# Performance work log

Hardware: AMD Instinct MI355X
Metric: run time of the kernel (lower is better)

## Reference

```python
import jax, jax.numpy as jnp
import numpy as np

B, N, D = 2, 1024, 1024
H, DH = 16, 64          # nhead, head_dim (D = H*DH)
FF = 4096               # dim_feedforward = 4*D
E = 8                   # num experts
EPS = 1e-5


def layer_norm(x, s, b):
    m = jnp.mean(x, -1, keepdims=True)
    v = jnp.mean((x - m) ** 2, -1, keepdims=True)
    return (x - m) * jax.lax.rsqrt(v + EPS) * s + b


def moe_gate(x, Wg):
    # top-1 gating: expert index + gate probability per token
    probs = jax.nn.softmax(x @ Wg, axis=-1)            # [B,N,E]
    idx = jnp.argmax(probs, axis=-1)                   # [B,N]
    gw = jnp.take_along_axis(probs, idx[..., None], -1)[..., 0]  # [B,N]
    return idx, gw


def moe_linear(x, W, b, idx, gw):
    # x:[B,N,Din], W:[E,Din,Dout], b:[E,Dout]; route each token to expert idx
    y = jnp.einsum('bnd,edh->bneh', x, W) + b          # [B,N,E,Dout]
    oh = jax.nn.one_hot(idx, E, dtype=x.dtype)         # [B,N,E]
    return jnp.einsum('bneh,bne->bnh', y, oh) * gw[..., None]


def setup_inputs() -> dict:
    key = jax.random.key(0)
    ks = jax.random.split(key, 8)
    g = lambda k, shape, sc: jax.random.normal(k, shape, jnp.float32) * sc
    inv_d = 1.0 / np.sqrt(D)
    return dict(
        src=g(ks[0], (B, N, D), 1.0),
        key_padding_mask=jnp.zeros((B, N), dtype=bool),
        Wg_attn=g(ks[1], (D, E), inv_d),
        Wqkv=g(ks[2], (E, D, 3 * D), inv_d), bqkv=jnp.zeros((E, 3 * D), jnp.float32),
        Wo=g(ks[3], (E, D, D), inv_d), bo=jnp.zeros((E, D), jnp.float32),
        Wg_ffn=g(ks[4], (D, E), inv_d),
        W1=g(ks[5], (E, D, FF), inv_d), b1=jnp.zeros((E, FF), jnp.float32),
        W2=g(ks[6], (E, FF, D), 1.0 / np.sqrt(FF)), b2=jnp.zeros((E, D), jnp.float32),
        ln1_s=jnp.ones((D,), jnp.float32), ln1_b=jnp.zeros((D,), jnp.float32),
        ln2_s=jnp.ones((D,), jnp.float32), ln2_b=jnp.zeros((D,), jnp.float32),
    )


def reference(src, key_padding_mask, Wg_attn, Wqkv, bqkv, Wo, bo,
              Wg_ffn, W1, b1, W2, b2, ln1_s, ln1_b, ln2_s, ln2_b):
    # attention mask: key_padding_mask.unsqueeze(1).unsqueeze(1) * -10000
    mask = jnp.where(key_padding_mask[:, None, None, :], -10000.0, 0.0).astype(src.dtype)

    # --- MoE self-attention (gate decided once, reused for qkv and dense) ---
    idx, gw = moe_gate(src, Wg_attn)
    qkv = moe_linear(src, Wqkv, bqkv, idx, gw)                 # [B,N,3D]
    q, k, v = jnp.split(qkv, 3, axis=-1)
    heads = lambda t: t.reshape(B, N, H, DH).transpose(0, 2, 1, 3)  # [B,H,N,DH]
    q, k, v = heads(q), heads(k), heads(v)
    scores = jnp.einsum('bhqd,bhkd->bhqk', q, k) / np.sqrt(DH) + mask
    probs = jax.nn.softmax(scores, axis=-1)
    ctx = jnp.einsum('bhqk,bhkd->bhqd', probs, v)
    ctx = ctx.transpose(0, 2, 1, 3).reshape(B, N, D)
    attn_out = moe_linear(ctx, Wo, bo, idx, gw)

    # post-norm residual
    x = layer_norm(src + attn_out, ln1_s, ln1_b)

    # --- MoE FFN (its own gate, shared across both linears) ---
    fidx, fgw = moe_gate(x, Wg_ffn)
    h = jax.nn.gelu(moe_linear(x, W1, b1, fidx, fgw))
    ffn = moe_linear(h, W2, b2, fidx, fgw)

    return layer_norm(x + ffn, ln2_s, ln2_b)
```

## Files before the change

### kernel.cpp

```cpp
#include <hip/hip_runtime.h>


#define B_   2
#define N_   1024
#define D_   1024
#define H_   16
#define DH_  64
#define FF_  4096
#define E_   8
#define NTOK 2048

typedef __attribute__((ext_vector_type(8))) short short8;
typedef __attribute__((ext_vector_type(8))) unsigned short ushort8;
typedef __attribute__((ext_vector_type(4))) unsigned short ushort4v;
typedef __attribute__((ext_vector_type(4))) float f32x4;
typedef __attribute__((ext_vector_type(2))) unsigned int uint32x2;

__device__ inline unsigned short f2bf(float f) {
  unsigned u = __float_as_uint(f);
  u += 0x7FFFu + ((u >> 16) & 1u);
  return (unsigned short)(u >> 16);
}

__device__ inline float gelu_tanh(float x) {
  float x3 = x * x * x;
  float t = tanhf(0.7978845608028654f * (x + 0.044715f * x3));
  return 0.5f * x * (1.0f + t);
}

__global__ __launch_bounds__(256) void gate_kernel(
    const float* __restrict__ X, const float* __restrict__ Wg,
    int* __restrict__ idx, float* __restrict__ gwv, int* __restrict__ cnt) {
  int t = blockIdx.x * 4 + (threadIdx.x >> 6);
  int lane = threadIdx.x & 63;
  const float* x = X + (size_t)t * D_;
  float acc[E_];
#pragma unroll
  for (int j = 0; j < E_; j++) acc[j] = 0.f;
#pragma unroll
  for (int i = 0; i < 16; i++) {
    int d = i * 64 + lane;
    float xv = x[d];
    const float4* w = (const float4*)(Wg + (size_t)d * E_);
    float4 w0 = w[0], w1 = w[1];
    acc[0] += xv * w0.x; acc[1] += xv * w0.y; acc[2] += xv * w0.z; acc[3] += xv * w0.w;
    acc[4] += xv * w1.x; acc[5] += xv * w1.y; acc[6] += xv * w1.z; acc[7] += xv * w1.w;
  }
#pragma unroll
  for (int o = 1; o < 64; o <<= 1) {
#pragma unroll
    for (int j = 0; j < E_; j++) acc[j] += __shfl_xor(acc[j], o, 64);
  }
  float m = acc[0]; int bi = 0;
#pragma unroll
  for (int j = 1; j < E_; j++) { if (acc[j] > m) { m = acc[j]; bi = j; } }
  float den = 0.f;
#pragma unroll
  for (int j = 0; j < E_; j++) den += expf(acc[j] - m);
  float gw = expf(acc[bi] - m) / den;
  if (lane == 0) { idx[t] = bi; gwv[t] = gw; atomicAdd(&cnt[bi], 1); }
}

__global__ __launch_bounds__(256) void route_kernel(
    const int* __restrict__ idx, const int* __restrict__ cnt,
    int* __restrict__ off, int* __restrict__ perm, int ntok) {
  __shared__ int loff[E_ + 1];
  __shared__ int lfill[E_];
  if (threadIdx.x == 0) {
    int s = 0;
    for (int e = 0; e < E_; e++) { loff[e] = s; s += cnt[e]; }
    loff[E_] = s;
  }
  if (threadIdx.x < E_) lfill[threadIdx.x] = 0;
  __syncthreads();
  for (int t = (int)threadIdx.x; t < ntok; t += 256) {
    int e = idx[t];
    int p = atomicAdd(&lfill[e], 1);
    perm[loff[e] + p] = t;
  }
  if (threadIdx.x < E_ + 1) off[threadIdx.x] = loff[threadIdx.x];
}

__global__ __launch_bounds__(256) void cast_bf16_kernel(
    const float* __restrict__ in, unsigned short* __restrict__ out) {
  size_t i = ((size_t)blockIdx.x * 256 + threadIdx.x) * 8;
  float4 v0 = *(const float4*)(in + i);
  float4 v1 = *(const float4*)(in + i + 4);
  ushort8 o;
  o[0] = f2bf(v0.x); o[1] = f2bf(v0.y); o[2] = f2bf(v0.z); o[3] = f2bf(v0.w);
  o[4] = f2bf(v1.x); o[5] = f2bf(v1.y); o[6] = f2bf(v1.z); o[7] = f2bf(v1.w);
  *(ushort8*)(out + i) = o;
}

template <int KS>
__global__ __launch_bounds__(256, 3) void gemm_kernel(
    const unsigned short* __restrict__ A, int ldA,
    const float* __restrict__ W,
    const int* __restrict__ perm, const int* __restrict__ off,
    float* __restrict__ part, int K, int N) {
  __shared__ __align__(16) unsigned short As[128][32];
  __shared__ __align__(16) unsigned short Bs[128][40];
  __shared__ int toks[128];

  int e = blockIdx.y;
  int base = off[e];
  int cnt = off[e + 1] - base;
  int mt = blockIdx.z / KS;
  int kc = blockIdx.z % KS;
  int m0 = mt * 128;
  if (m0 >= cnt) return;
  int rows_valid = min(128, cnt - m0);
  int tid = threadIdx.x;
  if (tid < 128) {
    int r = (tid < rows_valid) ? tid : (rows_valid - 1);
    toks[tid] = perm[base + m0 + r];
  }
  int nb = blockIdx.x * 128;
  int lane = tid & 63, wave = tid >> 6;
  int wm = (wave & 1) * 64, wn = (wave >> 1) * 64;
  int lr = lane & 15, lg = lane >> 4;
  int aswz = (lg ^ ((lr >> 1) & 3)) << 3;
  int bswz = (lg ^ ((lr >> 2) & 3)) << 3;

  f32x4 acc[4][4];
#pragma unroll
  for (int m = 0; m < 4; m++)
#pragma unroll
    for (int n = 0; n < 4; n++) acc[m][n] = (f32x4){0.f, 0.f, 0.f, 0.f};

  int arow = tid >> 1;
  int aj0 = (tid & 1) * 2;
  int as_ = (arow >> 1) & 3;
  int k4 = (tid & 7) * 4, n0 = (tid >> 3) * 4;

  int KL = K / KS, kbeg = kc * KL;
  int nt = KL / 32;
  __syncthreads();

  const unsigned short* abase = A + (size_t)toks[arow] * ldA + aj0 * 8;
  const float* wbase = W + ((size_t)e * K + k4) * N + nb + n0;

  ushort8 aR0, aR1;
  f32x4 bA0, bA1, bA2, bA3, bB0, bB1, bB2, bB3;

#define LOAD_A(KK) {                                                      \
    const unsigned short* ap = abase + (KK);                              \
    aR0 = *(const ushort8*)ap;                                            \
    aR1 = *(const ushort8*)(ap + 8); }

#define LOAD_B(KK, R0, R1, R2, R3) {                                      \
    const float* wp = wbase + (size_t)(KK) * N;                           \
    R0 = *(const f32x4*)wp;                                               \
    R1 = *(const f32x4*)(wp + N);                                         \
    R2 = *(const f32x4*)(wp + 2 * N);                                     \
    R3 = *(const f32x4*)(wp + 3 * N); }

#define PUBLISH(R0, R1, R2, R3) {                                         \
    *(ushort8*)&As[arow][(aj0 ^ as_) << 3] = aR0;                         \
    *(ushort8*)&As[arow][((aj0 + 1) ^ as_) << 3] = aR1;                   \
    _Pragma("unroll")                                                     \
    for (int j = 0; j < 4; j++) {                                         \
      int n = n0 + j;                                                     \
      int bb = (((k4 >> 3) ^ ((n >> 2) & 3)) << 3) | (k4 & 7);            \
      unsigned lo = (unsigned)f2bf(R0[j]) | ((unsigned)f2bf(R1[j]) << 16);\
      unsigned hi = (unsigned)f2bf(R2[j]) | ((unsigned)f2bf(R3[j]) << 16);\
      *(uint32x2*)&Bs[n][bb] = (uint32x2){lo, hi};                        \
    } }

#define COMPUTE() {                                                       \
    short8 av[4], bv[4];                                                  \
    _Pragma("unroll")                                                     \
    for (int m = 0; m < 4; m++)                                           \
      av[m] = *(const short8*)&As[wm + m * 16 + lr][aswz];                \
    _Pragma("unroll")                                                     \
    for (int n = 0; n < 4; n++)                                           \
      bv[n] = *(const short8*)&Bs[wn + n * 16 + lr][bswz];                \
    __builtin_amdgcn_s_setprio(1);                                        \
    _Pragma("unroll")                                                     \
    for (int n = 0; n < 4; n++)                                           \
      _Pragma("unroll")                                                   \
      for (int m = 0; m < 4; m++)                                         \
        acc[m][n] = __builtin_amdgcn_mfma_f32_16x16x32_bf16(              \
            av[m], bv[n], acc[m][n], 0, 0, 0);                            \
    __builtin_amdgcn_s_setprio(0); }

  LOAD_A(kbeg);
  LOAD_B(kbeg, bA0, bA1, bA2, bA3);
  if (nt > 1) LOAD_B(kbeg + 32, bB0, bB1, bB2, bB3);

  for (int t = 0; t < nt; t += 2) {
    int k0 = kbeg + t * 32;
    PUBLISH(bA0, bA1, bA2, bA3);
    if (t + 1 < nt) LOAD_A(k0 + 32);
    if (t + 2 < nt) LOAD_B(k0 + 64, bA0, bA1, bA2, bA3);
    asm volatile("s_waitcnt lgkmcnt(0)" ::: "memory");
    __builtin_amdgcn_s_barrier();
    COMPUTE();
    __builtin_amdgcn_s_barrier();
    if (t + 1 < nt) {
      PUBLISH(bB0, bB1, bB2, bB3);
      if (t + 2 < nt) LOAD_A(k0 + 64);
      if (t + 3 < nt) LOAD_B(k0 + 96, bB0, bB1, bB2, bB3);
      asm volatile("s_waitcnt lgkmcnt(0)" ::: "memory");
      __builtin_amdgcn_s_barrier();
      COMPUTE();
      __builtin_amdgcn_s_barrier();
    }
  }
#undef LOAD_A
#undef LOAD_B
#undef PUBLISH
#undef COMPUTE

  float* pr = part + (size_t)kc * ((size_t)NTOK * N);
#pragma unroll
  for (int n = 0; n < 4; n++) {
    int col = nb + wn + n * 16 + lr;
#pragma unroll
    for (int m = 0; m < 4; m++) {
#pragma unroll
      for (int reg = 0; reg < 4; reg++) {
        int r = wm + m * 16 + lg * 4 + reg;
        if (r < rows_valid)
          pr[(size_t)toks[r] * N + col] = acc[m][n][reg];
      }
    }
  }
}

template <int KS, bool GELU, bool OBF16>
__global__ __launch_bounds__(256) void reduce_kernel(
    const float* __restrict__ part, const float* __restrict__ bias,
    const float* __restrict__ gwv, const int* __restrict__ idx,
    void* __restrict__ out, int N) {
  int t = blockIdx.y;
  int n = (blockIdx.x * 256 + threadIdx.x) * 4;
  int e = idx[t];
  float gw = gwv[t];
  const float* p = part + (size_t)t * N + n;
  float4 a = *(const float4*)p;
#pragma unroll
  for (int k = 1; k < KS; k++) {
    float4 q = *(const float4*)(p + (size_t)k * NTOK * N);
    a.x += q.x; a.y += q.y; a.z += q.z; a.w += q.w;
  }
  float4 bv = *(const float4*)(bias + (size_t)e * N + n);
  a.x = (a.x + bv.x) * gw; a.y = (a.y + bv.y) * gw;
  a.z = (a.z + bv.z) * gw; a.w = (a.w + bv.w) * gw;
  if constexpr (GELU) {
    a.x = gelu_tanh(a.x); a.y = gelu_tanh(a.y);
    a.z = gelu_tanh(a.z); a.w = gelu_tanh(a.w);
  }
  if constexpr (OBF16) {
    ushort4v o;
    o[0] = f2bf(a.x); o[1] = f2bf(a.y); o[2] = f2bf(a.z); o[3] = f2bf(a.w);
    *(ushort4v*)((unsigned short*)out + (size_t)t * N + n) = o;
  } else {
    *(float4*)((float*)out + (size_t)t * N + n) = a;
  }
}

__global__ __launch_bounds__(256) void vtrans_kernel(
    const unsigned short* __restrict__ qkv, unsigned short* __restrict__ vT) {
  __shared__ __align__(16) unsigned short T[64][72];
  int bh = blockIdx.x;
  int b = bh >> 4, h = bh & 15;
  int tile = blockIdx.y;
  int tid = threadIdx.x;
  {
    int tk = tid >> 2, dof = (tid & 3) * 16;
    const unsigned short* p =
        qkv + ((size_t)(b * N_ + tile * 64 + tk)) * 3072 + 2048 + h * 64 + dof;
    *(ushort8*)&T[tk][dof] = *(const ushort8*)p;
    *(ushort8*)&T[tk][dof + 8] = *(const ushort8*)(p + 8);
  }
  __syncthreads();
  {
    int dh = tid >> 2, tof = (tid & 3) * 16;
    ushort8 o0, o1;
#pragma unroll
    for (int i = 0; i < 8; i++) o0[i] = T[tof + i][dh];
#pragma unroll
    for (int i = 0; i < 8; i++) o1[i] = T[tof + 8 + i][dh];
    unsigned short* q = vT + ((size_t)bh * 64 + dh) * N_ + tile * 64 + tof;
    *(ushort8*)q = o0;
    *(ushort8*)(q + 8) = o1;
  }
}

__global__ __launch_bounds__(256) void attn_kernel(
    const unsigned short* __restrict__ qkv, const unsigned short* __restrict__ vT,
    const unsigned char* __restrict__ kpm, unsigned short* __restrict__ ctx) {
  __shared__ __align__(16) unsigned short Qs[64][72];
  __shared__ __align__(16) unsigned short Ks[64][72];
  __shared__ __align__(16) unsigned short Vs[64][72];
  __shared__ __align__(16) unsigned short Ps[4][16][72];
  __shared__ float maskf[64];
  int qt = blockIdx.x, bh = blockIdx.y;
  int b = bh >> 4, h = bh & 15;
  int tid = threadIdx.x, lane = tid & 63, wave = tid >> 6;
  int lr = lane & 15, lg = lane >> 4;
  {
    int r = tid >> 2, dof = (tid & 3) * 16;
    const unsigned short* p = qkv + ((size_t)(b * N_ + qt * 64 + r)) * 3072 + h * 64 + dof;
    *(ushort8*)&Qs[r][dof] = *(const ushort8*)p;
    *(ushort8*)&Qs[r][dof + 8] = *(const ushort8*)(p + 8);
  }
  __syncthreads();
  short8 aq[2];
  aq[0] = *(const short8*)&Qs[wave * 16 + lr][lg * 8];
  aq[1] = *(const short8*)&Qs[wave * 16 + lr][32 + lg * 8];
  f32x4 O[4];
  float mrun[4], lrun[4];
#pragma unroll
  for (int r = 0; r < 4; r++) { mrun[r] = -1e30f; lrun[r] = 0.f; O[r] = (f32x4){0.f, 0.f, 0.f, 0.f}; }

  for (int kt = 0; kt < 16; kt++) {
    __syncthreads();
    {
      int r = tid >> 2, dof = (tid & 3) * 16;
      const unsigned short* p =
          qkv + ((size_t)(b * N_ + kt * 64 + r)) * 3072 + 1024 + h * 64 + dof;
      *(ushort8*)&Ks[r][dof] = *(const ushort8*)p;
      *(ushort8*)&Ks[r][dof + 8] = *(const ushort8*)(p + 8);
      const unsigned short* pv = vT + ((size_t)bh * 64 + r) * N_ + kt * 64 + dof;
      *(ushort8*)&Vs[r][dof] = *(const ushort8*)pv;
      *(ushort8*)&Vs[r][dof + 8] = *(const ushort8*)(pv + 8);
      if (tid < 64) maskf[tid] = kpm[b * N_ + kt * 64 + tid] ? -10000.f : 0.f;
    }
    __syncthreads();
    f32x4 S[4];
#pragma unroll
    for (int n = 0; n < 4; n++) {
      f32x4 s = (f32x4){0.f, 0.f, 0.f, 0.f};
#pragma unroll
      for (int ks = 0; ks < 2; ks++) {
        short8 bk = *(const short8*)&Ks[n * 16 + lr][ks * 32 + lg * 8];
        s = __builtin_amdgcn_mfma_f32_16x16x32_bf16(aq[ks], bk, s, 0, 0, 0);
      }
      float mv = maskf[n * 16 + lr];
#pragma unroll
      for (int r = 0; r < 4; r++) s[r] = s[r] * 0.125f + mv;
      S[n] = s;
    }
    float cur[4];
#pragma unroll
    for (int r = 0; r < 4; r++)
      cur[r] = fmaxf(fmaxf(S[0][r], S[1][r]), fmaxf(S[2][r], S[3][r]));
#pragma unroll
    for (int o = 1; o < 16; o <<= 1) {
#pragma unroll
      for (int r = 0; r < 4; r++) cur[r] = fmaxf(cur[r], __shfl_xor(cur[r], o, 64));
    }
    float alpha[4], rsum[4];
#pragma unroll
    for (int r = 0; r < 4; r++) {
      float mn = fmaxf(mrun[r], cur[r]);
      alpha[r] = expf(mrun[r] - mn);
      mrun[r] = mn;
      rsum[r] = 0.f;
    }
#pragma unroll
    for (int n = 0; n < 4; n++) {
#pragma unroll
      for (int r = 0; r < 4; r++) {
        S[n][r] = expf(S[n][r] - mrun[r]);
        rsum[r] += S[n][r];
      }
    }
#pragma unroll
    for (int o = 1; o < 16; o <<= 1) {
#pragma unroll
      for (int r = 0; r < 4; r++) rsum[r] += __shfl_xor(rsum[r], o, 64);
    }
#pragma unroll
    for (int r = 0; r < 4; r++) lrun[r] = lrun[r] * alpha[r] + rsum[r];
#pragma unroll
    for (int d = 0; d < 4; d++)
#pragma unroll
      for (int r = 0; r < 4; r++) O[d][r] *= alpha[r];
#pragma unroll
    for (int n = 0; n < 4; n++)
#pragma unroll
      for (int r = 0; r < 4; r++) Ps[wave][lg * 4 + r][n * 16 + lr] = f2bf(S[n][r]);
    short8 pf[2];
    pf[0] = *(const short8*)&Ps[wave][lr][lg * 8];
    pf[1] = *(const short8*)&Ps[wave][lr][32 + lg * 8];
#pragma unroll
    for (int d = 0; d < 4; d++) {
#pragma unroll
      for (int ks = 0; ks < 2; ks++) {
        short8 bv = *(const short8*)&Vs[d * 16 + lr][ks * 32 + lg * 8];
        O[d] = __builtin_amdgcn_mfma_f32_16x16x32_bf16(pf[ks], bv, O[d], 0, 0, 0);
      }
    }
  }
#pragma unroll
  for (int r = 0; r < 4; r++) lrun[r] = 1.f / lrun[r];
#pragma unroll
  for (int d = 0; d < 4; d++) {
#pragma unroll
    for (int r = 0; r < 4; r++) {
      int q = qt * 64 + wave * 16 + lg * 4 + r;
      int dh = d * 16 + lr;
      ctx[((size_t)(b * N_ + q)) * D_ + h * DH_ + dh] = f2bf(O[d][r] * lrun[r]);
    }
  }
}

template <int KS, bool WBF>
__global__ __launch_bounds__(256) void ln_reduce_kernel(
    const float* __restrict__ res, const float* __restrict__ part,
    const float* __restrict__ bias, const float* __restrict__ gwv,
    const int* __restrict__ idx,
    const float* __restrict__ S, const float* __restrict__ Bi,
    float* __restrict__ O, unsigned short* __restrict__ Obf) {
  int t = blockIdx.x, tid = threadIdx.x;
  int e = idx[t];
  float gw = gwv[t];
  const float* p = part + (size_t)t * D_ + tid * 4;
  float4 a = *(const float4*)p;
#pragma unroll
  for (int k = 1; k < KS; k++) {
    float4 q = *(const float4*)(p + (size_t)k * NTOK * D_);
    a.x += q.x; a.y += q.y; a.z += q.z; a.w += q.w;
  }
  float4 bv4 = *(const float4*)(bias + (size_t)e * D_ + tid * 4);
  float4 vr = ((const float4*)(res + (size_t)t * D_))[tid];
  float4 v;
  v.x = vr.x + (a.x + bv4.x) * gw;
  v.y = vr.y + (a.y + bv4.y) * gw;
  v.z = vr.z + (a.z + bv4.z) * gw;
  v.w = vr.w + (a.w + bv4.w) * gw;
  float s = v.x + v.y + v.z + v.w;
  float sq = v.x * v.x + v.y * v.y + v.z * v.z + v.w * v.w;
#pragma unroll
  for (int o = 1; o < 64; o <<= 1) {
    s += __shfl_xor(s, o, 64);
    sq += __shfl_xor(sq, o, 64);
  }
  __shared__ float ss[4], ssq[4];
  int wave = tid >> 6, lane = tid & 63;
  if (lane == 0) { ss[wave] = s; ssq[wave] = sq; }
  __syncthreads();
  float ts = ss[0] + ss[1] + ss[2] + ss[3];
  float tsq = ssq[0] + ssq[1] + ssq[2] + ssq[3];
  float mean = ts * (1.f / D_);
  float var = tsq * (1.f / D_) - mean * mean;
  float rs = rsqrtf(var + 1e-5f);
  float4 sv = ((const float4*)S)[tid];
  float4 bi = ((const float4*)Bi)[tid];
  float4 o;
  o.x = (v.x - mean) * rs * sv.x + bi.x;
  o.y = (v.y - mean) * rs * sv.y + bi.y;
  o.z = (v.z - mean) * rs * sv.z + bi.z;
  o.w = (v.w - mean) * rs * sv.w + bi.w;
  ((float4*)(O + (size_t)t * D_))[tid] = o;
  if constexpr (WBF) {
    ushort4v ob;
    ob[0] = f2bf(o.x); ob[1] = f2bf(o.y); ob[2] = f2bf(o.z); ob[3] = f2bf(o.w);
    *(ushort4v*)(Obf + (size_t)t * D_ + tid * 4) = ob;
  }
}

extern "C" void kernel_launch(void* const* d_in, const int* in_sizes, int n_in,
                              void* d_out, int out_size, void* d_ws, size_t ws_size,
                              hipStream_t stream) {
  (void)in_sizes; (void)n_in; (void)out_size; (void)ws_size;
  const float* src     = (const float*)d_in[0];
  const unsigned char* kpm = (const unsigned char*)d_in[1];
  const float* Wg_attn = (const float*)d_in[2];
  const float* Wqkv    = (const float*)d_in[3];
  const float* bqkv    = (const float*)d_in[4];
  const float* Wo      = (const float*)d_in[5];
  const float* bo      = (const float*)d_in[6];
  const float* Wg_ffn  = (const float*)d_in[7];
  const float* W1      = (const float*)d_in[8];
  const float* b1      = (const float*)d_in[9];
  const float* W2      = (const float*)d_in[10];
  const float* b2      = (const float*)d_in[11];
  const float* ln1_s   = (const float*)d_in[12];
  const float* ln1_b   = (const float*)d_in[13];
  const float* ln2_s   = (const float*)d_in[14];
  const float* ln2_b   = (const float*)d_in[15];
  float* out = (float*)d_out;

  char* ws = (char*)d_ws;
  size_t o = 0;
  auto alloc = [&](size_t bytes) -> void* {
    void* p = ws + o;
    o += (bytes + 255) & ~(size_t)255;
    return p;
  };
  int* meta = (int*)alloc(256);
  int* cnt1 = meta;
  int* off1 = meta + 8;
  int* cnt2 = meta + 17;
  int* off2 = meta + 25;
  int* idx1 = (int*)alloc(NTOK * 4);
  float* gw1 = (float*)alloc(NTOK * 4);
  int* perm1 = (int*)alloc(NTOK * 4);
  int* idx2 = (int*)alloc(NTOK * 4);
  float* gw2 = (float*)alloc(NTOK * 4);
  int* perm2 = (int*)alloc(NTOK * 4);
  unsigned short* qkvb = (unsigned short*)alloc((size_t)NTOK * 3072 * 2);
  unsigned short* vT = (unsigned short*)alloc((size_t)32 * 64 * N_ * 2);
  unsigned short* hbuf = qkvb;
  unsigned short* ctx = (unsigned short*)alloc((size_t)NTOK * D_ * 2);
  unsigned short* src_bf = ctx;
  unsigned short* x_bf = ctx;
  float* x = (float*)alloc((size_t)NTOK * D_ * 4);
  float* part = (float*)alloc((size_t)2 * NTOK * FF_ * 4);

  hipMemsetAsync(meta, 0, 256, stream);

  cast_bf16_kernel<<<1024, 256, 0, stream>>>(src, src_bf);
  gate_kernel<<<512, 256, 0, stream>>>(src, Wg_attn, idx1, gw1, cnt1);
  route_kernel<<<1, 256, 0, stream>>>(idx1, cnt1, off1, perm1, NTOK);
  gemm_kernel<2><<<dim3(3072 / 128, 8, 32), 256, 0, stream>>>(
      src_bf, 1024, Wqkv, perm1, off1, part, 1024, 3072);
  reduce_kernel<2, false, true><<<dim3(3, NTOK), 256, 0, stream>>>(
      part, bqkv, gw1, idx1, qkvb, 3072);
  vtrans_kernel<<<dim3(32, 16), 256, 0, stream>>>(qkvb, vT);
  attn_kernel<<<dim3(16, 32), 256, 0, stream>>>(qkvb, vT, kpm, ctx);
  gemm_kernel<4><<<dim3(1024 / 128, 8, 64), 256, 0, stream>>>(
      ctx, 1024, Wo, perm1, off1, part, 1024, 1024);
  ln_reduce_kernel<4, true><<<NTOK, 256, 0, stream>>>(
      src, part, bo, gw1, idx1, ln1_s, ln1_b, x, x_bf);

  gate_kernel<<<512, 256, 0, stream>>>(x, Wg_ffn, idx2, gw2, cnt2);
  route_kernel<<<1, 256, 0, stream>>>(idx2, cnt2, off2, perm2, NTOK);
  gemm_kernel<2><<<dim3(4096 / 128, 8, 32), 256, 0, stream>>>(
      x_bf, 1024, W1, perm2, off2, part, 1024, 4096);
  reduce_kernel<2, true, true><<<dim3(4, NTOK), 256, 0, stream>>>(
      part, b1, gw2, idx2, hbuf, 4096);
  gemm_kernel<4><<<dim3(8, 8, 64), 256, 0, stream>>>(
      hbuf, 4096, W2, perm2, off2, part, 4096, 1024);
  ln_reduce_kernel<4, false><<<NTOK, 256, 0, stream>>>(
      x, part, b2, gw2, idx2, ln2_s, ln2_b, out, (unsigned short*)nullptr);
}
```

Measured before the change: 698.9 us.

## Fuse bias/gate/GELU epilogue into MoE GEMM and enlarge M tile to 256

The grouped expert GEMM now uses 512-thread blocks with a 256-row M tile. Half the threads load A rows and the other half load and convert the fp32 weights, which are still converted to bf16 on the fly. For the QKV and FFN1 GEMMs, split-K is removed and bias, gate scaling and GELU are applied in the GEMM epilogue with a direct bf16 write, which eliminates the separate reduce kernels and their fp32 partial-buffer traffic. The Wo and W2 GEMMs drop from split-K 4 to 2. The intent is to cut kernel launches and memory traffic and to reuse each converted weight tile across more rows. The cost is fewer blocks in flight and possible underfill when an expert has few tokens.

After: 653.5 us. -6.5%, faster.

```diff
diff --git a/kernel.cpp b/kernel.cpp
--- a/kernel.cpp
+++ b/kernel.cpp
@@ -92,32 +92,36 @@
   *(ushort8*)(out + i) = o;
 }
 
-template <int KS>
-__global__ __launch_bounds__(256, 3) void gemm_kernel(
+template <int KS, int EPI>
+__global__ __launch_bounds__(512, 2) void gemm_kernel(
     const unsigned short* __restrict__ A, int ldA,
     const float* __restrict__ W,
+    const float* __restrict__ bias, const float* __restrict__ gwv,
     const int* __restrict__ perm, const int* __restrict__ off,
-    float* __restrict__ part, int K, int N) {
-  __shared__ __align__(16) unsigned short As[128][32];
+    void* __restrict__ outp, int K, int N) {
+  __shared__ __align__(16) unsigned short As[256][32];
   __shared__ __align__(16) unsigned short Bs[128][40];
-  __shared__ int toks[128];
+  __shared__ int toks[256];
+  __shared__ float gws[256];
 
   int e = blockIdx.y;
   int base = off[e];
   int cnt = off[e + 1] - base;
   int mt = blockIdx.z / KS;
   int kc = blockIdx.z % KS;
-  int m0 = mt * 128;
+  int m0 = mt * 256;
   if (m0 >= cnt) return;
-  int rows_valid = min(128, cnt - m0);
+  int rows_valid = min(256, cnt - m0);
   int tid = threadIdx.x;
-  if (tid < 128) {
+  if (tid < 256) {
     int r = (tid < rows_valid) ? tid : (rows_valid - 1);
-    toks[tid] = perm[base + m0 + r];
+    int tk = perm[base + m0 + r];
+    toks[tid] = tk;
+    gws[tid] = gwv[tk];
   }
   int nb = blockIdx.x * 128;
   int lane = tid & 63, wave = tid >> 6;
-  int wm = (wave & 1) * 64, wn = (wave >> 1) * 64;
+  int wm = (wave & 3) * 64, wn = (wave >> 2) * 64;
   int lr = lane & 15, lg = lane >> 4;
   int aswz = (lg ^ ((lr >> 1) & 3)) << 3;
   int bswz = (lg ^ ((lr >> 2) & 3)) << 3;
@@ -128,27 +132,30 @@
 #pragma unroll
     for (int n = 0; n < 4; n++) acc[m][n] = (f32x4){0.f, 0.f, 0.f, 0.f};
 
-  int arow = tid >> 1;
-  int aj0 = (tid & 1) * 2;
+  bool isB = tid < 256;
+  int c = tid & 31, rq = (tid >> 5) & 7;
+  int k4 = rq * 4, n0 = c * 4;
+  int arow = tid & 255;
   int as_ = (arow >> 1) & 3;
-  int k4 = (tid & 7) * 4, n0 = (tid >> 3) * 4;
 
   int KL = K / KS, kbeg = kc * KL;
   int nt = KL / 32;
   __syncthreads();
 
-  const unsigned short* abase = A + (size_t)toks[arow] * ldA + aj0 * 8;
+  const unsigned short* abase = A + (size_t)toks[arow] * ldA;
   const float* wbase = W + ((size_t)e * K + k4) * N + nb + n0;
 
-  ushort8 aR0, aR1;
+  ushort8 aR0, aR1, aR2, aR3;
   f32x4 bA0, bA1, bA2, bA3, bB0, bB1, bB2, bB3;
 
-#define LOAD_A(KK) {                                                      \
+#define LOAD_A(KK) if (!isB) {                                            \
     const unsigned short* ap = abase + (KK);                              \
     aR0 = *(const ushort8*)ap;                                            \
-    aR1 = *(const ushort8*)(ap + 8); }
-
-#define LOAD_B(KK, R0, R1, R2, R3) {                                      \
+    aR1 = *(const ushort8*)(ap + 8);                                      \
+    aR2 = *(const ushort8*)(ap + 16);                                     \
+    aR3 = *(const ushort8*)(ap + 24); }
+
+#define LOAD_B(KK, R0, R1, R2, R3) if (isB) {                             \
     const float* wp = wbase + (size_t)(KK) * N;                           \
     R0 = *(const f32x4*)wp;                                               \
     R1 = *(const f32x4*)(wp + N);                                         \
@@ -156,15 +163,20 @@
     R3 = *(const f32x4*)(wp + 3 * N); }
 
 #define PUBLISH(R0, R1, R2, R3) {                                         \
-    *(ushort8*)&As[arow][(aj0 ^ as_) << 3] = aR0;                         \
-    *(ushort8*)&As[arow][((aj0 + 1) ^ as_) << 3] = aR1;                   \
-    _Pragma("unroll")                                                     \
-    for (int j = 0; j < 4; j++) {                                         \
-      int n = n0 + j;                                                     \
-      int bb = (((k4 >> 3) ^ ((n >> 2) & 3)) << 3) | (k4 & 7);            \
-      unsigned lo = (unsigned)f2bf(R0[j]) | ((unsigned)f2bf(R1[j]) << 16);\
-      unsigned hi = (unsigned)f2bf(R2[j]) | ((unsigned)f2bf(R3[j]) << 16);\
-      *(uint32x2*)&Bs[n][bb] = (uint32x2){lo, hi};                        \
+    if (isB) {                                                            \
+      _Pragma("unroll")                                                   \
+      for (int j = 0; j < 4; j++) {                                       \
+        int n = n0 + j;                                                   \
+        int bb = (((k4 >> 3) ^ ((n >> 2) & 3)) << 3) | (k4 & 7);          \
+        unsigned lo = (unsigned)f2bf(R0[j]) | ((unsigned)f2bf(R1[j]) << 16);\
+        unsigned hi = (unsigned)f2bf(R2[j]) | ((unsigned)f2bf(R3[j]) << 16);\
+        *(uint32x2*)&Bs[n][bb] = (uint32x2){lo, hi};                      \
+      }                                                                   \
+    } else {                                                              \
+      *(ushort8*)&As[arow][(0 ^ as_) << 3] = aR0;                         \
+      *(ushort8*)&As[arow][(1 ^ as_) << 3] = aR1;                         \
+      *(ushort8*)&As[arow][(2 ^ as_) << 3] = aR2;                         \
+      *(ushort8*)&As[arow][(3 ^ as_) << 3] = aR3;                         \
     } }
 
 #define COMPUTE() {                                                       \
@@ -212,51 +224,43 @@
 #undef PUBLISH
 #undef COMPUTE
 
-  float* pr = part + (size_t)kc * ((size_t)NTOK * N);
-#pragma unroll
-  for (int n = 0; n < 4; n++) {
-    int col = nb + wn + n * 16 + lr;
-#pragma unroll
-    for (int m = 0; m < 4; m++) {
-#pragma unroll
-      for (int reg = 0; reg < 4; reg++) {
-        int r = wm + m * 16 + lg * 4 + reg;
-        if (r < rows_valid)
-          pr[(size_t)toks[r] * N + col] = acc[m][n][reg];
+  if constexpr (EPI == 0) {
+    float* pr = (float*)outp + (size_t)kc * ((size_t)NTOK * N);
+#pragma unroll
+    for (int n = 0; n < 4; n++) {
+      int col = nb + wn + n * 16 + lr;
+#pragma unroll
+      for (int m = 0; m < 4; m++) {
+#pragma unroll
+        for (int reg = 0; reg < 4; reg++) {
+          int r = wm + m * 16 + lg * 4 + reg;
+          if (r < rows_valid)
+            pr[(size_t)toks[r] * N + col] = acc[m][n][reg];
+        }
       }
     }
-  }
-}
-
-template <int KS, bool GELU, bool OBF16>
-__global__ __launch_bounds__(256) void reduce_kernel(
-    const float* __restrict__ part, const float* __restrict__ bias,
-    const float* __restrict__ gwv, const int* __restrict__ idx,
-    void* __restrict__ out, int N) {
-  int t = blockIdx.y;
-  int n = (blockIdx.x * 256 + threadIdx.x) * 4;
-  int e = idx[t];
-  float gw = gwv[t];
-  const float* p = part + (size_t)t * N + n;
-  float4 a = *(const float4*)p;
-#pragma unroll
-  for (int k = 1; k < KS; k++) {
-    float4 q = *(const float4*)(p + (size_t)k * NTOK * N);
-    a.x += q.x; a.y += q.y; a.z += q.z; a.w += q.w;
-  }
-  float4 bv = *(const float4*)(bias + (size_t)e * N + n);
-  a.x = (a.x + bv.x) * gw; a.y = (a.y + bv.y) * gw;
-  a.z = (a.z + bv.z) * gw; a.w = (a.w + bv.w) * gw;
-  if constexpr (GELU) {
-    a.x = gelu_tanh(a.x); a.y = gelu_tanh(a.y);
-    a.z = gelu_tanh(a.z); a.w = gelu_tanh(a.w);
-  }
-  if constexpr (OBF16) {
-    ushort4v o;
-    o[0] = f2bf(a.x); o[1] = f2bf(a.y); o[2] = f2bf(a.z); o[3] = f2bf(a.w);
-    *(ushort4v*)((unsigned short*)out + (size_t)t * N + n) = o;
   } else {
-    *(float4*)((float*)out + (size_t)t * N + n) = a;
+    unsigned short* po = (unsigned short*)outp;
+    float bcol[4];
+#pragma unroll
+    for (int n = 0; n < 4; n++)
+      bcol[n] = bias[(size_t)e * N + nb + wn + n * 16 + lr];
+#pragma unroll
+    for (int n = 0; n < 4; n++) {
+      int col = nb + wn + n * 16 + lr;
+#pragma unroll
+      for (int m = 0; m < 4; m++) {
+#pragma unroll
+        for (int reg = 0; reg < 4; reg++) {
+          int r = wm + m * 16 + lg * 4 + reg;
+          if (r < rows_valid) {
+            float v = (acc[m][n][reg] + bcol[n]) * gws[r];
+            if constexpr (EPI == 2) v = gelu_tanh(v);
+            po[(size_t)toks[r] * N + col] = f2bf(v);
+          }
+        }
+      }
+    }
   }
 }
 
@@ -510,32 +514,28 @@
   unsigned short* src_bf = ctx;
   unsigned short* x_bf = ctx;
   float* x = (float*)alloc((size_t)NTOK * D_ * 4);
-  float* part = (float*)alloc((size_t)2 * NTOK * FF_ * 4);
+  float* part = (float*)alloc((size_t)2 * NTOK * D_ * 4);
 
   hipMemsetAsync(meta, 0, 256, stream);
 
   cast_bf16_kernel<<<1024, 256, 0, stream>>>(src, src_bf);
   gate_kernel<<<512, 256, 0, stream>>>(src, Wg_attn, idx1, gw1, cnt1);
   route_kernel<<<1, 256, 0, stream>>>(idx1, cnt1, off1, perm1, NTOK);
-  gemm_kernel<2><<<dim3(3072 / 128, 8, 32), 256, 0, stream>>>(
-      src_bf, 1024, Wqkv, perm1, off1, part, 1024, 3072);
-  reduce_kernel<2, false, true><<<dim3(3, NTOK), 256, 0, stream>>>(
-      part, bqkv, gw1, idx1, qkvb, 3072);
+  gemm_kernel<1, 1><<<dim3(3072 / 128, 8, 8), 512, 0, stream>>>(
+      src_bf, 1024, Wqkv, bqkv, gw1, perm1, off1, qkvb, 1024, 3072);
   vtrans_kernel<<<dim3(32, 16), 256, 0, stream>>>(qkvb, vT);
   attn_kernel<<<dim3(16, 32), 256, 0, stream>>>(qkvb, vT, kpm, ctx);
-  gemm_kernel<4><<<dim3(1024 / 128, 8, 64), 256, 0, stream>>>(
-      ctx, 1024, Wo, perm1, off1, part, 1024, 1024);
-  ln_reduce_kernel<4, true><<<NTOK, 256, 0, stream>>>(
+  gemm_kernel<2, 0><<<dim3(1024 / 128, 8, 16), 512, 0, stream>>>(
+      ctx, 1024, Wo, bo, gw1, perm1, off1, part, 1024, 1024);
+  ln_reduce_kernel<2, true><<<NTOK, 256, 0, stream>>>(
       src, part, bo, gw1, idx1, ln1_s, ln1_b, x, x_bf);
 
   gate_kernel<<<512, 256, 0, stream>>>(x, Wg_ffn, idx2, gw2, cnt2);
   route_kernel<<<1, 256, 0, stream>>>(idx2, cnt2, off2, perm2, NTOK);
-  gemm_kernel<2><<<dim3(4096 / 128, 8, 32), 256, 0, stream>>>(
-      x_bf, 1024, W1, perm2, off2, part, 1024, 4096);
-  reduce_kernel<2, true, true><<<dim3(4, NTOK), 256, 0, stream>>>(
-      part, b1, gw2, idx2, hbuf, 4096);
-  gemm_kernel<4><<<dim3(8, 8, 64), 256, 0, stream>>>(
-      hbuf, 4096, W2, perm2, off2, part, 4096, 1024);
-  ln_reduce_kernel<4, false><<<NTOK, 256, 0, stream>>>(
+  gemm_kernel<1, 2><<<dim3(4096 / 128, 8, 8), 512, 0, stream>>>(
+      x_bf, 1024, W1, b1, gw2, perm2, off2, hbuf, 1024, 4096);
+  gemm_kernel<2, 0><<<dim3(1024 / 128, 8, 16), 512, 0, stream>>>(
+      hbuf, 4096, W2, b2, gw2, perm2, off2, part, 4096, 1024);
+  ln_reduce_kernel<2, false><<<NTOK, 256, 0, stream>>>(
       x, part, b2, gw2, idx2, ln2_s, ln2_b, out, (unsigned short*)nullptr);
 }
```
